# Kernel tuning notes

Measured on AMD Instinct MI355X. Metric: run time of the kernel, lower is better.

The kernel has to match this reference:

```python
import jax, jax.numpy as jnp
import numpy as np

H = 768          # hidden_size
NH = 12          # num heads
HD = H // NH     # head dim
NEG = -1e9       # stand-in for -inf masked_fill (numerically safe)


def setup_inputs() -> dict:
    key = jax.random.key(0)
    ks = jax.random.split(key, 8)
    B, T = 4, 2048
    s = 0.02
    return {
        "hidden_states": jax.random.normal(ks[0], (B, T, H), jnp.float32),
        "attention_mask": jnp.zeros((B, 1, 1, T), jnp.float32),
        "Wq": jax.random.normal(ks[1], (H, H), jnp.float32) * s,
        "bq": jnp.zeros((H,), jnp.float32),
        "Wk": jax.random.normal(ks[2], (H, H), jnp.float32) * s,
        "bk": jnp.zeros((H,), jnp.float32),
        "Wv": jax.random.normal(ks[3], (H, H), jnp.float32) * s,
        "bv": jnp.zeros((H,), jnp.float32),
    }


def _split_heads(x):
    b, t, _ = x.shape
    return x.reshape(b, t, NH, HD).transpose(0, 2, 1, 3)  # b h t d


def reference(hidden_states, attention_mask, Wq, bq, Wk, bk, Wv, bv):
    q = _split_heads(hidden_states @ Wq.T + bq)
    k = _split_heads(hidden_states @ Wk.T + bk)
    v = _split_heads(hidden_states @ Wv.T + bv)
    T = q.shape[2]
    scores = jnp.einsum('bhid,bhjd->bhij', q, k) / jnp.sqrt(jnp.float32(HD))
    causal = jnp.tril(jnp.ones((T, T), bool))
    scores = jnp.where(causal, scores, NEG) + attention_mask
    probs = jax.nn.softmax(scores, axis=-1)
    out = jnp.einsum('bhij,bhjd->bhid', probs, v)
    b = out.shape[0]
    return out.transpose(0, 2, 1, 3).reshape(b, T, H)  # b t (h d)
```

## Files before the change

kernel.cpp:

```cpp
#include <hip/hip_runtime.h>
#include <hip/hip_bf16.h>

#define Tsz 2048
#define Hsz 768
#define NHsz 12
#define HDsz 64

typedef unsigned short u16;
typedef unsigned int u32;
typedef __attribute__((ext_vector_type(8))) short bf16x8;
typedef __attribute__((ext_vector_type(4))) float f32x4;
typedef __attribute__((ext_vector_type(4))) u16 u16x4;

__device__ __forceinline__ u16 f2bf(float f) {
    union { __hip_bfloat16 h; u16 u; } c;
    c.h = __float2bfloat16(f);
    return c.u;
}

__device__ __forceinline__ void glds16(const void* src, void* ldsbase) {
    __builtin_amdgcn_global_load_lds(
        (const __attribute__((address_space(1))) u32*)src,
        (__attribute__((address_space(3))) u32*)ldsbase, 16, 0, 0);
}

#define BAR() do { asm volatile("" ::: "memory"); \
                   __builtin_amdgcn_s_barrier();  \
                   asm volatile("" ::: "memory"); } while (0)

#define LDSFRAG(base, row, c) \
    (*(const bf16x8*)((const char*)(base) + (row)*128 + ((((c) << 4)) ^ (((row) & 7) << 4))))

__global__ __launch_bounds__(256) void to_bf16(
    const float* __restrict__ X,
    const float* __restrict__ Wq, const float* __restrict__ Wk,
    const float* __restrict__ Wv,
    u16* __restrict__ xb, u16* __restrict__ wb)
{
    const int bx = blockIdx.x, tid = threadIdx.x;
    const float* src;
    u16* dst;
    size_t off;
    if (bx < 768) {
        src = X; dst = xb;
        off = ((size_t)bx * 256 + tid) * 32;
    } else {
        int r = bx - 768;
        int wsel = r / 72, lr = r % 72;
        src = (wsel == 0) ? Wq : (wsel == 1) ? Wk : Wv;
        dst = wb + (size_t)wsel * (Hsz * Hsz);
        off = ((size_t)lr * 256 + tid) * 32;
    }
    #pragma unroll
    for (int c = 0; c < 4; ++c) {
        float4 a = *(const float4*)(src + off + c * 8);
        float4 b = *(const float4*)(src + off + c * 8 + 4);
        bf16x8 v;
        v[0] = (short)f2bf(a.x); v[1] = (short)f2bf(a.y);
        v[2] = (short)f2bf(a.z); v[3] = (short)f2bf(a.w);
        v[4] = (short)f2bf(b.x); v[5] = (short)f2bf(b.y);
        v[6] = (short)f2bf(b.z); v[7] = (short)f2bf(b.w);
        *(bf16x8*)(dst + off + c * 8) = v;
    }
}

__global__ __launch_bounds__(256) void qkv_gemm(
    const u16* __restrict__ xb, const u16* __restrict__ wb,
    const float* __restrict__ bq, const float* __restrict__ bk,
    const float* __restrict__ bv,
    u16* __restrict__ q_ws, u16* __restrict__ k_ws, u16* __restrict__ vt_ws)
{
    const int tid = threadIdx.x;
    const int w = tid >> 6, l = tid & 63, lg = l >> 4, lh = l & 15;
    const int nb = blockIdx.x;
    const int m0 = blockIdx.y * 128;
    const int z = nb / 6;
    const int n0l = (nb % 6) * 128;
    const u16* Wb = wb + (size_t)z * (Hsz * Hsz);
    const float* bias = (z == 0) ? bq : (z == 1) ? bk : bv;

    __shared__ __align__(16) u16 Xs[2][128 * 64];
    __shared__ __align__(16) u16 Ws[2][128 * 64];

    const int wm = w >> 1, wn = w & 1;

    f32x4 acc[4][4];
    #pragma unroll
    for (int i = 0; i < 4; ++i)
        #pragma unroll
        for (int j = 0; j < 4; ++j)
            acc[i][j] = (f32x4){0.f, 0.f, 0.f, 0.f};

    auto stage = [&](int buf, int k0) {
        #pragma unroll
        for (int p = 0; p < 4; ++p) {
            int id = w * 256 + p * 64 + l;
            int r = id >> 3, c8 = id & 7;
            int cswz = c8 ^ (r & 7);
            glds16(xb + (size_t)(m0 + r) * Hsz + k0 + cswz * 8,
                   &Xs[buf][(w * 256 + p * 64) * 8]);
            glds16(Wb + (size_t)(n0l + r) * Hsz + k0 + cswz * 8,
                   &Ws[buf][(w * 256 + p * 64) * 8]);
        }
    };

    stage(0, 0);
    asm volatile("s_waitcnt vmcnt(0)" ::: "memory");
    BAR();

    #pragma unroll 1
    for (int ks = 0; ks < 12; ++ks) {
        const int cur = ks & 1;
        if (ks < 11) {
            stage(cur ^ 1, (ks + 1) * 64);
            asm volatile("s_waitcnt vmcnt(8)" ::: "memory");
        } else {
            asm volatile("s_waitcnt vmcnt(0)" ::: "memory");
        }
        BAR();

        __builtin_amdgcn_s_setprio(1);
        #pragma unroll
        for (int s = 0; s < 2; ++s) {
            bf16x8 af[4], bfr[4];
            #pragma unroll
            for (int tq = 0; tq < 4; ++tq) {
                af[tq]  = LDSFRAG(Xs[cur], wm * 64 + tq * 16 + lh, 4 * s + lg);
                bfr[tq] = LDSFRAG(Ws[cur], wn * 64 + tq * 16 + lh, 4 * s + lg);
            }
            #pragma unroll
            for (int mt = 0; mt < 4; ++mt)
                #pragma unroll
                for (int nt = 0; nt < 4; ++nt)
                    acc[mt][nt] = __builtin_amdgcn_mfma_f32_16x16x32_bf16(
                        af[mt], bfr[nt], acc[mt][nt], 0, 0, 0);
        }
        __builtin_amdgcn_s_setprio(0);
        BAR();
    }

    #pragma unroll
    for (int nt = 0; nt < 4; ++nt) {
        int nloc = n0l + wn * 64 + nt * 16 + lh;
        float bval = bias[nloc];
        int hh = nloc >> 6, d = nloc & 63;
        #pragma unroll
        for (int mt = 0; mt < 4; ++mt) {
            #pragma unroll
            for (int r = 0; r < 4; ++r) {
                int m = m0 + wm * 64 + mt * 16 + lg * 4 + r;
                int bb = m >> 11, t = m & 2047;
                u16 val = f2bf(acc[mt][nt][r] + bval);
                size_t bh = (size_t)(bb * NHsz + hh);
                if (z == 0)      q_ws[(bh * Tsz + t) * HDsz + d] = val;
                else if (z == 1) k_ws[(bh * Tsz + t) * HDsz + d] = val;
                else             vt_ws[(bh * HDsz + d) * Tsz + t] = val;
            }
        }
    }
}

__global__ __launch_bounds__(256) void attn_mfma(
    const u16* __restrict__ q_ws, const u16* __restrict__ k_ws,
    const u16* __restrict__ vt_ws, const float* __restrict__ am,
    float* __restrict__ out)
{
    const int tid = threadIdx.x;
    const int w = tid >> 6, l = tid & 63, lg = l >> 4, lh = l & 15;
    const int wg = blockIdx.x;
    const int swz = (wg & 7) * 96 + (wg >> 3);
    const int bx = swz & 15;
    const int grp = swz >> 4;
    const int h = grp % NHsz, b = grp / NHsz;
    const int bh = b * NHsz + h;

    const u16* Qb = q_ws + (size_t)bh * Tsz * HDsz;
    const u16* Kb = k_ws + (size_t)bh * Tsz * HDsz;
    const u16* Vb = vt_ws + (size_t)bh * HDsz * Tsz;
    const float* amb = am + (size_t)b * Tsz;

    __shared__ __align__(16) u16 Ks[2][64 * 64];
    __shared__ __align__(16) u16 Vs[2][64 * 64];
    __shared__ __align__(16) u16 Ps[4][16 * 64];
    __shared__ __align__(16) float ambs[Tsz];

    const float LOG2E  = 1.44269504f;
    const float SCALE2 = 0.125f * 1.44269504f;
    const f32x4 zero4 = {0.f, 0.f, 0.f, 0.f};
    u16* myP = &Ps[w][0];
    const int srcbase = l & 0x30;
    const int qo = lg * 4;

    #pragma unroll
    for (int i = 0; i < 2; ++i)
        glds16(amb + (size_t)(i * 256 + tid) * 4, ambs + (i * 256 + w * 64) * 4);
    asm volatile("s_waitcnt vmcnt(0)" ::: "memory");
    __syncthreads();
    #pragma unroll
    for (int i = 0; i < 8; ++i) ambs[tid * 8 + i] *= LOG2E;
    __syncthreads();

    #pragma unroll 1
    for (int ph = 0; ph < 2; ++ph) {
        const int qt = (ph == 0) ? (16 + bx) : (15 - bx);
        const int q0 = qt * 64 + w * 16;
        const int qrow = q0 + lh;

        #pragma unroll
        for (int p = 0; p < 2; ++p) {
            int id = w * 128 + p * 64 + l;
            int r = id >> 3, c8 = id & 7;
            int cswz = c8 ^ (r & 7);
            glds16(Kb + (size_t)r * HDsz + cswz * 8, &Ks[0][(w * 128 + p * 64) * 8]);
            glds16(Vb + (size_t)r * Tsz + cswz * 8, &Vs[0][(w * 128 + p * 64) * 8]);
        }
        bf16x8 qf0 = *(const bf16x8*)(Qb + (size_t)(q0 + lh) * HDsz + lg * 8);
        bf16x8 qf1 = *(const bf16x8*)(Qb + (size_t)(q0 + lh) * HDsz + lg * 8 + 32);
        asm volatile("s_waitcnt vmcnt(0)" ::: "memory");
        BAR();

        f32x4 o[4];
        #pragma unroll
        for (int n = 0; n < 4; ++n) o[n] = zero4;
        float m2 = -1e30f, l2 = 0.f;

        #pragma unroll 1
        for (int kt = 0; kt <= qt; ++kt) {
            const int cur = kt & 1;
            const int kv0 = kt * 64;

            if (kt < qt) {
                const int kv1 = kv0 + 64;
                #pragma unroll
                for (int p = 0; p < 2; ++p) {
                    int id = w * 128 + p * 64 + l;
                    int r = id >> 3, c8 = id & 7;
                    int cswz = c8 ^ (r & 7);
                    glds16(Kb + (size_t)(kv1 + r) * HDsz + cswz * 8,
                           &Ks[cur ^ 1][(w * 128 + p * 64) * 8]);
                    glds16(Vb + (size_t)r * Tsz + kv1 + cswz * 8,
                           &Vs[cur ^ 1][(w * 128 + p * 64) * 8]);
                }
                asm volatile("s_waitcnt vmcnt(4)" ::: "memory");
            } else {
                asm volatile("s_waitcnt vmcnt(0)" ::: "memory");
            }
            BAR();

            const u16* Ksb = &Ks[cur][0];
            const u16* Vsb = &Vs[cur][0];
            const bool diag = (kt == qt);

            f32x4 st[4];
            __builtin_amdgcn_s_setprio(1);
            if (!diag) {
                #pragma unroll
                for (int n = 0; n < 4; ++n) {
                    int row = n * 16 + lh;
                    bf16x8 kf0 = LDSFRAG(Ksb, row, lg);
                    bf16x8 kf1 = LDSFRAG(Ksb, row, 4 + lg);
                    f32x4 c = __builtin_amdgcn_mfma_f32_16x16x32_bf16(kf0, qf0, zero4, 0, 0, 0);
                    st[n] = __builtin_amdgcn_mfma_f32_16x16x32_bf16(kf1, qf1, c, 0, 0, 0);
                }
            } else {
                #pragma unroll
                for (int n = 0; n < 4; ++n) {
                    st[n] = zero4;
                    if (n <= w) {
                        int row = n * 16 + lh;
                        bf16x8 kf0 = LDSFRAG(Ksb, row, lg);
                        bf16x8 kf1 = LDSFRAG(Ksb, row, 4 + lg);
                        f32x4 c = __builtin_amdgcn_mfma_f32_16x16x32_bf16(kf0, qf0, zero4, 0, 0, 0);
                        st[n] = __builtin_amdgcn_mfma_f32_16x16x32_bf16(kf1, qf1, c, 0, 0, 0);
                    }
                }
            }
            __builtin_amdgcn_s_setprio(0);

            float pvv[16];
            float mx = -1e30f;
            if (!diag) {
                #pragma unroll
                for (int n = 0; n < 4; ++n) {
                    f32x4 a4 = *(const f32x4*)(ambs + kv0 + n * 16 + lg * 4);
                    #pragma unroll
                    for (int r = 0; r < 4; ++r) {
                        float sv = fmaf(st[n][r], SCALE2, a4[r]);
                        pvv[n * 4 + r] = sv;
                        mx = fmaxf(mx, sv);
                    }
                }
            } else {
                #pragma unroll
                for (int n = 0; n < 4; ++n) {
                    f32x4 a4 = *(const f32x4*)(ambs + kv0 + n * 16 + lg * 4);
                    #pragma unroll
                    for (int r = 0; r < 4; ++r) {
                        int kvj = kv0 + n * 16 + lg * 4 + r;
                        float sv = (kvj > qrow) ? -1e30f : fmaf(st[n][r], SCALE2, a4[r]);
                        pvv[n * 4 + r] = sv;
                        mx = fmaxf(mx, sv);
                    }
                }
            }
            mx = fmaxf(mx, __shfl_xor(mx, 16));
            mx = fmaxf(mx, __shfl_xor(mx, 32));

            const bool norescale = __all(mx <= m2 + 8.0f);
            float mn = m2;
            if (!norescale) mn = fmaxf(m2, mx);

            float ps = 0.f;
            #pragma unroll
            for (int i = 0; i < 16; ++i) {
                float p = exp2f(pvv[i] - mn);
                pvv[i] = p;
                ps += p;
            }
            ps += __shfl_xor(ps, 16);
            ps += __shfl_xor(ps, 32);

            if (norescale) {
                l2 += ps;
            } else {
                float corr = exp2f(m2 - mn);
                m2 = mn;
                l2 = l2 * corr + ps;
                float co[4];
                #pragma unroll
                for (int r = 0; r < 4; ++r)
                    co[r] = __shfl(corr, srcbase | (qo + r));
                #pragma unroll
                for (int n = 0; n < 4; ++n)
                    #pragma unroll
                    for (int r = 0; r < 4; ++r)
                        o[n][r] *= co[r];
            }

            #pragma unroll
            for (int n = 0; n < 4; ++n) {
                u16x4 v;
                v[0] = f2bf(pvv[n * 4 + 0]); v[1] = f2bf(pvv[n * 4 + 1]);
                v[2] = f2bf(pvv[n * 4 + 2]); v[3] = f2bf(pvv[n * 4 + 3]);
                int chunk = 2 * n + (lg >> 1);
                int byteoff = lh * 128 + ((chunk ^ (lh & 7)) << 4) + ((lg & 1) << 3);
                *(u16x4*)((char*)myP + byteoff) = v;
            }

            const int smaxv = (diag && w < 2) ? 0 : 1;
            __builtin_amdgcn_s_setprio(1);
            #pragma unroll
            for (int s = 0; s < 2; ++s) {
                if (s <= smaxv) {
                    int chunk = (4 * s + lg) ^ (lh & 7);
                    bf16x8 pf = *(const bf16x8*)((const char*)myP + lh * 128 + (chunk << 4));
                    #pragma unroll
                    for (int n = 0; n < 4; ++n) {
                        bf16x8 vf = LDSFRAG(Vsb, n * 16 + lh, 4 * s + lg);
                        o[n] = __builtin_amdgcn_mfma_f32_16x16x32_bf16(pf, vf, o[n], 0, 0, 0);
                    }
                }
            }
            __builtin_amdgcn_s_setprio(0);
            BAR();
        }

        float linv[4];
        #pragma unroll
        for (int r = 0; r < 4; ++r)
            linv[r] = 1.0f / __shfl(l2, srcbase | (qo + r));
        float* ob = out + ((size_t)(b * Tsz + q0 + qo)) * Hsz + h * HDsz + lh;
        #pragma unroll
        for (int r = 0; r < 4; ++r)
            #pragma unroll
            for (int n = 0; n < 4; ++n)
                ob[r * Hsz + n * 16] = o[n][r] * linv[r];
    }
}

extern "C" void kernel_launch(void* const* d_in, const int* in_sizes, int n_in,
                              void* d_out, int out_size, void* d_ws, size_t ws_size,
                              hipStream_t stream) {
    const float* X  = (const float*)d_in[0];
    const float* am = (const float*)d_in[1];
    const float* Wq = (const float*)d_in[2];
    const float* bq = (const float*)d_in[3];
    const float* Wk = (const float*)d_in[4];
    const float* bk = (const float*)d_in[5];
    const float* Wv = (const float*)d_in[6];
    const float* bv = (const float*)d_in[7];
    float* out = (float*)d_out;

    const size_t per = (size_t)8192 * Hsz;
    u16* q_ws  = (u16*)d_ws;
    u16* k_ws  = q_ws + per;
    u16* vt_ws = k_ws + per;

    u16* xb = (u16*)d_out;
    u16* wb = xb + per;

    to_bf16<<<dim3(984), 256, 0, stream>>>(X, Wq, Wk, Wv, xb, wb);

    dim3 g1(18, 64);
    qkv_gemm<<<g1, 256, 0, stream>>>(xb, wb, bq, bk, bv, q_ws, k_ws, vt_ws);

    attn_mfma<<<dim3(768), 256, 0, stream>>>(q_ws, k_ws, vt_ws, am, out);
}
```

Before: 148.0 us.

## Load V fragments directly to registers and vectorize QKV projection stores

```diff
diff --git a/kernel.cpp b/kernel.cpp
--- a/kernel.cpp
+++ b/kernel.cpp
@@ -128,39 +128,63 @@
                 af[tq]  = LDSFRAG(Xs[cur], wm * 64 + tq * 16 + lh, 4 * s + lg);
                 bfr[tq] = LDSFRAG(Ws[cur], wn * 64 + tq * 16 + lh, 4 * s + lg);
             }
-            #pragma unroll
-            for (int mt = 0; mt < 4; ++mt)
-                #pragma unroll
-                for (int nt = 0; nt < 4; ++nt)
-                    acc[mt][nt] = __builtin_amdgcn_mfma_f32_16x16x32_bf16(
-                        af[mt], bfr[nt], acc[mt][nt], 0, 0, 0);
+            if (z <= 1) {
+                #pragma unroll
+                for (int mt = 0; mt < 4; ++mt)
+                    #pragma unroll
+                    for (int nt = 0; nt < 4; ++nt)
+                        acc[mt][nt] = __builtin_amdgcn_mfma_f32_16x16x32_bf16(
+                            bfr[nt], af[mt], acc[mt][nt], 0, 0, 0);
+            } else {
+                #pragma unroll
+                for (int mt = 0; mt < 4; ++mt)
+                    #pragma unroll
+                    for (int nt = 0; nt < 4; ++nt)
+                        acc[mt][nt] = __builtin_amdgcn_mfma_f32_16x16x32_bf16(
+                            af[mt], bfr[nt], acc[mt][nt], 0, 0, 0);
+            }
         }
         __builtin_amdgcn_s_setprio(0);
         BAR();
     }
 
-    #pragma unroll
-    for (int nt = 0; nt < 4; ++nt) {
-        int nloc = n0l + wn * 64 + nt * 16 + lh;
-        float bval = bias[nloc];
-        int hh = nloc >> 6, d = nloc & 63;
+    if (z <= 1) {
+        u16* outp = (z == 0) ? q_ws : k_ws;
         #pragma unroll
         for (int mt = 0; mt < 4; ++mt) {
-            #pragma unroll
-            for (int r = 0; r < 4; ++r) {
-                int m = m0 + wm * 64 + mt * 16 + lg * 4 + r;
-                int bb = m >> 11, t = m & 2047;
-                u16 val = f2bf(acc[mt][nt][r] + bval);
-                size_t bh = (size_t)(bb * NHsz + hh);
-                if (z == 0)      q_ws[(bh * Tsz + t) * HDsz + d] = val;
-                else if (z == 1) k_ws[(bh * Tsz + t) * HDsz + d] = val;
-                else             vt_ws[(bh * HDsz + d) * Tsz + t] = val;
+            int m = m0 + wm * 64 + mt * 16 + lh;
+            int bb = m >> 11, t = m & 2047;
+            #pragma unroll
+            for (int nt = 0; nt < 4; ++nt) {
+                int nbase = n0l + wn * 64 + nt * 16 + lg * 4;
+                int hh = nbase >> 6, d0 = nbase & 63;
+                f32x4 b4 = *(const f32x4*)(bias + nbase);
+                u16x4 pk;
+                #pragma unroll
+                for (int r = 0; r < 4; ++r) pk[r] = f2bf(acc[mt][nt][r] + b4[r]);
+                *(u16x4*)(outp + ((size_t)(bb * NHsz + hh) * Tsz + t) * HDsz + d0) = pk;
+            }
+        }
+    } else {
+        #pragma unroll
+        for (int nt = 0; nt < 4; ++nt) {
+            int nloc = n0l + wn * 64 + nt * 16 + lh;
+            float bval = bias[nloc];
+            int hh = nloc >> 6, d = nloc & 63;
+            #pragma unroll
+            for (int mt = 0; mt < 4; ++mt) {
+                int t0m = m0 + wm * 64 + mt * 16 + lg * 4;
+                int bb = t0m >> 11, t0 = t0m & 2047;
+                u16x4 pk;
+                #pragma unroll
+                for (int r = 0; r < 4; ++r) pk[r] = f2bf(acc[mt][nt][r] + bval);
+                *(u16x4*)(vt_ws + ((size_t)(bb * NHsz + hh) * HDsz + d) * Tsz + t0) = pk;
             }
         }
     }
 }
 
-__global__ __launch_bounds__(256) void attn_mfma(
+__global__ __launch_bounds__(256, 4) void attn_mfma(
     const u16* __restrict__ q_ws, const u16* __restrict__ k_ws,
     const u16* __restrict__ vt_ws, const float* __restrict__ am,
     float* __restrict__ out)
@@ -180,7 +204,6 @@
     const float* amb = am + (size_t)b * Tsz;
 
     __shared__ __align__(16) u16 Ks[2][64 * 64];
-    __shared__ __align__(16) u16 Vs[2][64 * 64];
     __shared__ __align__(16) u16 Ps[4][16 * 64];
     __shared__ __align__(16) float ambs[Tsz];
 
@@ -212,12 +235,9 @@
             int r = id >> 3, c8 = id & 7;
             int cswz = c8 ^ (r & 7);
             glds16(Kb + (size_t)r * HDsz + cswz * 8, &Ks[0][(w * 128 + p * 64) * 8]);
-            glds16(Vb + (size_t)r * Tsz + cswz * 8, &Vs[0][(w * 128 + p * 64) * 8]);
         }
         bf16x8 qf0 = *(const bf16x8*)(Qb + (size_t)(q0 + lh) * HDsz + lg * 8);
         bf16x8 qf1 = *(const bf16x8*)(Qb + (size_t)(q0 + lh) * HDsz + lg * 8 + 32);
-        asm volatile("s_waitcnt vmcnt(0)" ::: "memory");
-        BAR();
 
         f32x4 o[4];
         #pragma unroll
@@ -228,6 +248,14 @@
         for (int kt = 0; kt <= qt; ++kt) {
             const int cur = kt & 1;
             const int kv0 = kt * 64;
+
+            bf16x8 vfr[8];
+            #pragma unroll
+            for (int s = 0; s < 2; ++s)
+                #pragma unroll
+                for (int n = 0; n < 4; ++n)
+                    vfr[s * 4 + n] = *(const bf16x8*)(
+                        Vb + (size_t)(n * 16 + lh) * Tsz + kv0 + (4 * s + lg) * 8);
 
             if (kt < qt) {
                 const int kv1 = kv0 + 64;
@@ -238,17 +266,14 @@
                     int cswz = c8 ^ (r & 7);
                     glds16(Kb + (size_t)(kv1 + r) * HDsz + cswz * 8,
                            &Ks[cur ^ 1][(w * 128 + p * 64) * 8]);
-                    glds16(Vb + (size_t)r * Tsz + kv1 + cswz * 8,
-                           &Vs[cur ^ 1][(w * 128 + p * 64) * 8]);
-                }
-                asm volatile("s_waitcnt vmcnt(4)" ::: "memory");
+                }
+                asm volatile("s_waitcnt vmcnt(10)" ::: "memory");
             } else {
-                asm volatile("s_waitcnt vmcnt(0)" ::: "memory");
+                asm volatile("s_waitcnt vmcnt(8)" ::: "memory");
             }
             BAR();
 
             const u16* Ksb = &Ks[cur][0];
-            const u16* Vsb = &Vs[cur][0];
             const bool diag = (kt == qt);
 
             f32x4 st[4];
@@ -276,6 +301,7 @@
                 }
             }
             __builtin_amdgcn_s_setprio(0);
+            BAR();
 
             float pvv[16];
             float mx = -1e30f;
@@ -347,6 +373,9 @@
                 *(u16x4*)((char*)myP + byteoff) = v;
             }
 
+            if (kt < qt) asm volatile("s_waitcnt vmcnt(2)" ::: "memory");
+            else         asm volatile("s_waitcnt vmcnt(0)" ::: "memory");
+
             const int smaxv = (diag && w < 2) ? 0 : 1;
             __builtin_amdgcn_s_setprio(1);
             #pragma unroll
@@ -355,14 +384,12 @@
                     int chunk = (4 * s + lg) ^ (lh & 7);
                     bf16x8 pf = *(const bf16x8*)((const char*)myP + lh * 128 + (chunk << 4));
                     #pragma unroll
-                    for (int n = 0; n < 4; ++n) {
-                        bf16x8 vf = LDSFRAG(Vsb, n * 16 + lh, 4 * s + lg);
-                        o[n] = __builtin_amdgcn_mfma_f32_16x16x32_bf16(pf, vf, o[n], 0, 0, 0);
-                    }
+                    for (int n = 0; n < 4; ++n)
+                        o[n] = __builtin_amdgcn_mfma_f32_16x16x32_bf16(
+                            pf, vfr[s * 4 + n], o[n], 0, 0, 0);
                 }
             }
             __builtin_amdgcn_s_setprio(0);
-            BAR();
         }
 
         float linv[4];
```

New measurement: 172.1 us. 16.3% more time.
